# Optimization experiments

Measured on AMD Instinct MI355X. Metric: run time of the kernel, lower is better.

## Reference

```python
import jax, jax.numpy as jnp
import numpy as np

D_IN = 1024
D_OUT = 1024
NUM_HEADS = 16
HEAD_DIM = D_OUT // NUM_HEADS
SEQ = 2048
BATCH = 2


def setup_inputs() -> dict:
    key = jax.random.key(0)
    ks = jax.random.split(key, 6)
    s = 1.0 / np.sqrt(D_IN)
    x = jax.random.normal(ks[0], (BATCH, SEQ, D_IN), dtype=jnp.float32)
    Wq = jax.random.uniform(ks[1], (D_IN, D_OUT), jnp.float32, -s, s)
    Wk = jax.random.uniform(ks[2], (D_IN, D_OUT), jnp.float32, -s, s)
    Wv = jax.random.uniform(ks[3], (D_IN, D_OUT), jnp.float32, -s, s)
    Wo = jax.random.uniform(ks[4], (D_OUT, D_OUT), jnp.float32, -s, s)
    bo = jax.random.uniform(ks[5], (D_OUT,), jnp.float32, -s, s)
    return {"x": x, "Wq": Wq, "Wk": Wk, "Wv": Wv, "Wo": Wo, "bo": bo}


def reference(x, Wq, Wk, Wv, Wo, bo):
    b, n, _ = x.shape
    # projections, split into heads: (b, h, n, hd)
    def split_heads(t):
        return t.reshape(b, n, NUM_HEADS, HEAD_DIM).transpose(0, 2, 1, 3)
    q = split_heads(x @ Wq)
    k = split_heads(x @ Wk)
    v = split_heads(x @ Wv)
    scores = jnp.einsum("bhqd,bhkd->bhqk", q, k)
    causal = jnp.triu(jnp.ones((n, n), dtype=bool), k=1)
    scores = jnp.where(causal, -jnp.inf, scores)
    attn = jax.nn.softmax(scores / np.sqrt(HEAD_DIM), axis=-1)
    # dropout prob is 0.0 -> identity
    ctx = jnp.einsum("bhqk,bhkd->bhqd", attn, v)
    ctx = ctx.transpose(0, 2, 1, 3).reshape(b, n, D_OUT)
    return ctx @ Wo + bo
```

## Files before the change

kernel.cpp:

```cpp
#include <hip/hip_runtime.h>
#include <hip/hip_bf16.h>
#include <stdint.h>

#define D_IN   1024
#define D_OUT  1024
#define NHEAD  16
#define HDIM   64
#define SEQ    2048
#define BATCH  2
#define M_TOT  (BATCH*SEQ)

typedef __attribute__((ext_vector_type(8)))  short bfx8;
typedef __attribute__((ext_vector_type(4)))  short bfx4;
typedef __attribute__((ext_vector_type(4)))  float fx4;
typedef __attribute__((ext_vector_type(16))) float fx16;
typedef unsigned short u16;
typedef unsigned int   u32;

__device__ __forceinline__ u16 f2bf(float f) {
    u32 u = __builtin_bit_cast(u32, f);
    u32 r = (u + 0x7FFFu + ((u >> 16) & 1u)) >> 16;
    return (u16)r;
}

__device__ __forceinline__ u32 cvtpk(float lo, float hi) {
    u32 r;
    asm("v_cvt_pk_bf16_f32 %0, %1, %2" : "=v"(r) : "v"(lo), "v"(hi));
    return r;
}

__device__ __forceinline__ void gload16(const u16* g, u16* l) {
    __builtin_amdgcn_global_load_lds(
        (const __attribute__((address_space(1))) void*)g,
        (__attribute__((address_space(3))) void*)l, 16, 0, 0);
}

__global__ void k_conv_x(const float* __restrict__ x, u16* __restrict__ xb) {
    int i = blockIdx.x * 256 + threadIdx.x;
    const float4* s = reinterpret_cast<const float4*>(x);
    float4 a = s[2*i], b = s[2*i+1];
    uint4 o;
    o.x = (u32)f2bf(a.x) | ((u32)f2bf(a.y) << 16);
    o.y = (u32)f2bf(a.z) | ((u32)f2bf(a.w) << 16);
    o.z = (u32)f2bf(b.x) | ((u32)f2bf(b.y) << 16);
    o.w = (u32)f2bf(b.z) | ((u32)f2bf(b.w) << 16);
    reinterpret_cast<uint4*>(xb)[i] = o;
}

__global__ void k_conv_wt(const float* __restrict__ Wq, const float* __restrict__ Wk,
                          const float* __restrict__ Wv, const float* __restrict__ Wo,
                          u16* __restrict__ wt) {
    __shared__ float tile[32][33];
    int wsel = blockIdx.z;
    const float* W = (wsel == 0) ? Wq : (wsel == 1) ? Wk : (wsel == 2) ? Wv : Wo;
    const float scale = (wsel == 0) ? 0.125f : 1.0f;
    u16* dst = wt + (size_t)wsel * D_IN * D_OUT;
    int r0 = blockIdx.y * 32, c0 = blockIdx.x * 32;
    int tx = threadIdx.x & 31, ty = threadIdx.x >> 5;
    #pragma unroll
    for (int k = 0; k < 4; k++) {
        int i = ty + k * 8;
        tile[i][tx] = W[(size_t)(r0 + i) * D_OUT + c0 + tx];
    }
    __syncthreads();
    #pragma unroll
    for (int k = 0; k < 4; k++) {
        int i = ty + k * 8;
        dst[(size_t)(c0 + i) * D_IN + r0 + tx] = f2bf(tile[tx][i] * scale);
    }
}

template<int MODE>
__global__ __launch_bounds__(256) void k_gemm128(const u16* __restrict__ A,
                                                 const u16* __restrict__ Bt,
                                                 const float* __restrict__ bias,
                                                 u16* __restrict__ outb,
                                                 float* __restrict__ outf) {
    __shared__ u16 aL[128][32];
    __shared__ u16 bL[128][32];
    const int K = 1024;
    const int nb = blockIdx.x * 128, mb = blockIdx.y * 128;
    const int t = threadIdx.x, lane = t & 63, w = t >> 6;
    const int wr = w >> 1, wc = w & 1;
    const int li = lane & 15, lg = lane >> 4;
    const int srow = lane >> 2, schunk = (lane & 3) * 8;

    fx4 acc[4][4];
    #pragma unroll
    for (int i = 0; i < 4; i++)
        #pragma unroll
        for (int j = 0; j < 4; j++) acc[i][j] = fx4{0.f, 0.f, 0.f, 0.f};

    const u16* aBase = A  + (size_t)(mb + w * 32 + srow) * K + schunk;
    const u16* bBase = Bt + (size_t)(nb + w * 32 + srow) * K + schunk;

    for (int kb = 0; kb < K; kb += 32) {
        #pragma unroll
        for (int c = 0; c < 2; c++) {
            gload16(aBase + (size_t)c * 16 * K + kb, &aL[w * 32 + c * 16][0]);
            gload16(bBase + (size_t)c * 16 * K + kb, &bL[w * 32 + c * 16][0]);
        }
        __syncthreads();
        bfx8 af[4], bf[4];
        #pragma unroll
        for (int mi = 0; mi < 4; mi++)
            af[mi] = *reinterpret_cast<const bfx8*>(&aL[wr * 64 + mi * 16 + li][lg * 8]);
        #pragma unroll
        for (int ni = 0; ni < 4; ni++)
            bf[ni] = *reinterpret_cast<const bfx8*>(&bL[wc * 64 + ni * 16 + li][lg * 8]);
        #pragma unroll
        for (int mi = 0; mi < 4; mi++)
            #pragma unroll
            for (int ni = 0; ni < 4; ni++)
                acc[mi][ni] = __builtin_amdgcn_mfma_f32_16x16x32_bf16(af[mi], bf[ni], acc[mi][ni], 0, 0, 0);
        __syncthreads();
    }

    #pragma unroll
    for (int mi = 0; mi < 4; mi++) {
        #pragma unroll
        for (int ni = 0; ni < 4; ni++) {
            const int n = nb + wc * 64 + ni * 16 + li;
            const int m0 = mb + wr * 64 + mi * 16 + lg * 4;
            if (MODE == 0) {
                const int proj = n >> 10, h = (n >> 6) & 15, d = n & 63;
                const int b = m0 >> 11, s0 = m0 & 2047;
                if (proj == 2) {
                    u16* op = outb + (size_t)2 * M_TOT * D_OUT +
                              ((size_t)(b * NHEAD + h) * HDIM + d) * SEQ + s0;
                    bfx4 pk = {(short)f2bf(acc[mi][ni][0]), (short)f2bf(acc[mi][ni][1]),
                               (short)f2bf(acc[mi][ni][2]), (short)f2bf(acc[mi][ni][3])};
                    *reinterpret_cast<bfx4*>(op) = pk;
                } else {
                    u16* op = outb + (size_t)proj * M_TOT * D_OUT;
                    #pragma unroll
                    for (int r = 0; r < 4; r++)
                        op[((size_t)(b * NHEAD + h) * SEQ + s0 + r) * HDIM + d] =
                            f2bf(acc[mi][ni][r]);
                }
            } else {
                const float bv = bias[n];
                #pragma unroll
                for (int r = 0; r < 4; r++)
                    outf[(size_t)(m0 + r) * D_OUT + n] = acc[mi][ni][r] + bv;
            }
        }
    }
}

__global__ __launch_bounds__(128, 2) void k_attn(const u16* __restrict__ Q,
                                                 const u16* __restrict__ Kp,
                                                 const u16* __restrict__ Vt,
                                                 u16* __restrict__ ctx) {
    __shared__ u16 kbuf[2][64][64];
    __shared__ u16 vbuf[2][64][64];

    const int g    = blockIdx.x;
    const int pid  = g & 255, half = g >> 8;
    const int bh   = pid & 31, jb = pid >> 5;
    const int qi   = (half == 0) ? jb : (half == 1) ? (31 - jb)
                   : (half == 2) ? (8 + jb) : (23 - jb);
    const int ntk  = qi + 1;

    const size_t base = (size_t)bh * SEQ * HDIM;
    const int t = threadIdx.x, lane = t & 63, w = t >> 6;
    const int l31 = lane & 31, hi = lane >> 5;
    const int srow = lane >> 3;
    const int ts = (lane & 7) ^ srow;
    const int bq = bh >> 4, hh = bh & 15;
    const int swz = (l31 & 7) * 8;
    const int qwb = qi * 64 + w * 32;
    const int qg  = qwb + l31;

    auto stage = [&](int bi, int kvb) {
        #pragma unroll
        for (int i = 0; i < 4; i++) {
            const int rb = w * 32 + i * 8;
            const int rr = rb + srow;
            gload16(Kp + base + (size_t)(kvb + rr) * HDIM + ts * 8, &kbuf[bi][rb][0]);
            gload16(Vt + base + (size_t)rr * SEQ + kvb + ts * 8,    &vbuf[bi][rb][0]);
        }
    };

    bfx8 qf[4];
    #pragma unroll
    for (int dc = 0; dc < 4; dc++)
        qf[dc] = *reinterpret_cast<const bfx8*>(
            &Q[base + (size_t)qg * HDIM + dc * 16 + hi * 8]);
    fx16 cacc[2];
    #pragma unroll
    for (int dt = 0; dt < 2; dt++)
        #pragma unroll
        for (int r = 0; r < 16; r++) cacc[dt][r] = 0.f;
    float lsum = 0.f;

    stage(0, 0);

    for (int ti = 0; ti < ntk; ti++) {
        if (ti + 1 < ntk) {
            stage((ti + 1) & 1, (ti + 1) * 64);
            asm volatile("s_waitcnt vmcnt(8)" ::: "memory");
        } else {
            asm volatile("s_waitcnt vmcnt(0)" ::: "memory");
        }
        __builtin_amdgcn_s_barrier();
        __builtin_amdgcn_sched_barrier(0);
        const int bi = ti & 1, kvb = ti * 64;
        fx16 sc[2];
        #pragma unroll
        for (int s = 0; s < 2; s++) {
            #pragma unroll
            for (int r = 0; r < 16; r++) sc[s][r] = 0.f;
            #pragma unroll
            for (int dc = 0; dc < 4; dc++) {
                bfx8 kf = *reinterpret_cast<const bfx8*>(
                    &kbuf[bi][s * 32 + l31][(dc * 16 + hi * 8) ^ swz]);
                sc[s] = __builtin_amdgcn_mfma_f32_32x32x16_bf16(kf, qf[dc], sc[s], 0, 0, 0);
            }
        }
        if (kvb + 63 > qwb) {
            #pragma unroll
            for (int s = 0; s < 2; s++)
                #pragma unroll
                for (int r = 0; r < 16; r++) {
                    int kvg = kvb + s * 32 + (r & 3) + 8 * (r >> 2) + 4 * hi;
                    if (kvg > qg) sc[s][r] = -1e30f;
                }
        }
        float ps = 0.f;
        #pragma unroll
        for (int s = 0; s < 2; s++)
            #pragma unroll
            for (int r = 0; r < 16; r++) {
                float pv = __expf(sc[s][r]);
                sc[s][r] = pv;
                ps += pv;
            }
        lsum += ps;
        #pragma unroll
        for (int c = 0; c < 4; c++) {
            const int s = c >> 1, rb = (c & 1) * 8;
            u32 a0 = cvtpk(sc[s][rb + 0], sc[s][rb + 1]);
            u32 a1 = cvtpk(sc[s][rb + 2], sc[s][rb + 3]);
            u32 b0 = cvtpk(sc[s][rb + 4], sc[s][rb + 5]);
            u32 b1 = cvtpk(sc[s][rb + 6], sc[s][rb + 7]);
            u32 X0 = hi ? a0 : b0, X1 = hi ? a1 : b1;
            u32 Y0 = (u32)__shfl_xor((int)X0, 32);
            u32 Y1 = (u32)__shfl_xor((int)X1, 32);
            uint4 pw;
            pw.x = hi ? Y0 : a0;
            pw.y = hi ? Y1 : a1;
            pw.z = hi ? b0 : Y0;
            pw.w = hi ? b1 : Y1;
            bfx8 pf = __builtin_bit_cast(bfx8, pw);
            #pragma unroll
            for (int dt = 0; dt < 2; dt++) {
                bfx8 vf = *reinterpret_cast<const bfx8*>(
                    &vbuf[bi][dt * 32 + l31][(c * 16 + hi * 8) ^ swz]);
                cacc[dt] = __builtin_amdgcn_mfma_f32_32x32x16_bf16(pf, vf, cacc[dt], 0, 0, 0);
            }
        }
        asm volatile("s_waitcnt lgkmcnt(0)" ::: "memory");
        __builtin_amdgcn_s_barrier();
    }

    float ltot = lsum + __shfl_xor(lsum, 32);
    float linv = 1.0f / ltot;
    #pragma unroll
    for (int r = 0; r < 16; r++) {
        const int qpat = (r & 3) + 8 * (r >> 2) + 4 * hi;
        float rl = __shfl(linv, qpat);
        const int q = qwb + qpat;
        #pragma unroll
        for (int dt = 0; dt < 2; dt++)
            ctx[((size_t)(bq * SEQ + q)) * D_OUT + hh * HDIM + dt * 32 + l31] =
                f2bf(cacc[dt][r] * rl);
    }
}

extern "C" void kernel_launch(void* const* d_in, const int* in_sizes, int n_in,
                              void* d_out, int out_size, void* d_ws, size_t ws_size,
                              hipStream_t stream) {
    const float* x  = (const float*)d_in[0];
    const float* Wq = (const float*)d_in[1];
    const float* Wk = (const float*)d_in[2];
    const float* Wv = (const float*)d_in[3];
    const float* Wo = (const float*)d_in[4];
    const float* bo = (const float*)d_in[5];
    float* out = (float*)d_out;

    char* ws = (char*)d_ws;
    u16* xb   = (u16*)(ws);
    u16* wt   = (u16*)(ws + (8u << 20));
    u16* qkvb = (u16*)(ws + (16u << 20));
    u16* ctxb = (u16*)(ws + (40u << 20));

    const u16* Qb  = qkvb;
    const u16* Kb  = qkvb + (size_t)M_TOT * D_OUT;
    const u16* Vtb = qkvb + (size_t)2 * M_TOT * D_OUT;

    k_conv_x <<<2048, 256, 0, stream>>>(x, xb);
    k_conv_wt<<<dim3(32, 32, 4), 256, 0, stream>>>(Wq, Wk, Wv, Wo, wt);
    k_gemm128<0><<<dim3(24, 32), 256, 0, stream>>>(xb, wt, nullptr, qkvb, nullptr);
    k_attn   <<<dim3(1024), 128, 0, stream>>>(Qb, Kb, Vtb, ctxb);
    k_gemm128<1><<<dim3(8, 32), 256, 0, stream>>>(
        ctxb, wt + (size_t)3 * D_IN * D_OUT, bo, nullptr, out);
}
```

Baseline: 115.8 us.

## Split KV range of long causal query blocks into two partial blocks plus combine

Query blocks in the second half of the sequence (qi ≥ 16) now have their KV tiles split across two workgroups. The first part writes its unnormalised bf16 context into ctx and the second writes to a scratch buffer, each with its row sums. A new k_comb kernel adds the two partials and divides by the total sum. This caps per-block work at about 16 tiles to shorten the causal-imbalance tail. In exchange it adds a kernel launch, extra global traffic, and bf16 rounding of the unnormalised partials; the scratch buffers reuse the no-longer-needed xb workspace.

```diff
diff --git a/kernel.cpp b/kernel.cpp
--- a/kernel.cpp
+++ b/kernel.cpp
@@ -21,6 +21,10 @@
     u32 u = __builtin_bit_cast(u32, f);
     u32 r = (u + 0x7FFFu + ((u >> 16) & 1u)) >> 16;
     return (u16)r;
+}
+__device__ __forceinline__ float bf2f(u16 v) {
+    u32 u = (u32)v << 16;
+    return __builtin_bit_cast(float, u);
 }
 
 __device__ __forceinline__ u32 cvtpk(float lo, float hi) {
@@ -151,16 +155,32 @@
 __global__ __launch_bounds__(128, 2) void k_attn(const u16* __restrict__ Q,
                                                  const u16* __restrict__ Kp,
                                                  const u16* __restrict__ Vt,
-                                                 u16* __restrict__ ctx) {
+                                                 u16* __restrict__ ctx,
+                                                 u16* __restrict__ o1,
+                                                 float* __restrict__ l0,
+                                                 float* __restrict__ l1) {
     __shared__ u16 kbuf[2][64][64];
     __shared__ u16 vbuf[2][64][64];
 
-    const int g    = blockIdx.x;
-    const int pid  = g & 255, half = g >> 8;
-    const int bh   = pid & 31, jb = pid >> 5;
-    const int qi   = (half == 0) ? jb : (half == 1) ? (31 - jb)
-                   : (half == 2) ? (8 + jb) : (23 - jb);
-    const int ntk  = qi + 1;
+    const int g = blockIdx.x;
+    int qi, part, m;
+    const bool heavy = (g < 1024);
+    if (heavy) {
+        qi = 31 - (g >> 6);
+        part = (g >> 5) & 1;
+        m = g & 31;
+    } else {
+        int j = g - 1024;
+        qi = 15 - (j >> 5);
+        part = 0;
+        m = j & 31;
+    }
+    const int bh = (m & 7) * 4 + (m >> 3);
+    const int nt = qi + 1;
+    int t0, t1;
+    if (heavy) { int h1 = nt >> 1; t0 = part ? h1 : 0; t1 = part ? nt : h1; }
+    else       { t0 = 0; t1 = nt; }
+    const int ntL = t1 - t0;
 
     const size_t base = (size_t)bh * SEQ * HDIM;
     const int t = threadIdx.x, lane = t & 63, w = t >> 6;
@@ -194,18 +214,19 @@
         for (int r = 0; r < 16; r++) cacc[dt][r] = 0.f;
     float lsum = 0.f;
 
-    stage(0, 0);
-
-    for (int ti = 0; ti < ntk; ti++) {
-        if (ti + 1 < ntk) {
-            stage((ti + 1) & 1, (ti + 1) * 64);
+    stage(0, t0 * 64);
+
+    for (int tt = 0; tt < ntL; tt++) {
+        const int ti = t0 + tt;
+        if (tt + 1 < ntL) {
+            stage((tt + 1) & 1, (ti + 1) * 64);
             asm volatile("s_waitcnt vmcnt(8)" ::: "memory");
         } else {
             asm volatile("s_waitcnt vmcnt(0)" ::: "memory");
         }
         __builtin_amdgcn_s_barrier();
         __builtin_amdgcn_sched_barrier(0);
-        const int bi = ti & 1, kvb = ti * 64;
+        const int bi = tt & 1, kvb = ti * 64;
         fx16 sc[2];
         #pragma unroll
         for (int s = 0; s < 2; s++) {
@@ -265,17 +286,58 @@
     }
 
     float ltot = lsum + __shfl_xor(lsum, 32);
-    float linv = 1.0f / ltot;
-    #pragma unroll
-    for (int r = 0; r < 16; r++) {
-        const int qpat = (r & 3) + 8 * (r >> 2) + 4 * hi;
-        float rl = __shfl(linv, qpat);
-        const int q = qwb + qpat;
-        #pragma unroll
-        for (int dt = 0; dt < 2; dt++)
-            ctx[((size_t)(bq * SEQ + q)) * D_OUT + hh * HDIM + dt * 32 + l31] =
-                f2bf(cacc[dt][r] * rl);
-    }
+    if (!heavy) {
+        float linv = 1.0f / ltot;
+        #pragma unroll
+        for (int r = 0; r < 16; r++) {
+            const int qpat = (r & 3) + 8 * (r >> 2) + 4 * hi;
+            float rl = __shfl(linv, qpat);
+            const int q = qwb + qpat;
+            #pragma unroll
+            for (int dt = 0; dt < 2; dt++)
+                ctx[((size_t)(bq * SEQ + q)) * D_OUT + hh * HDIM + dt * 32 + l31] =
+                    f2bf(cacc[dt][r] * rl);
+        }
+    } else {
+        const int qi16 = qi - 16;
+        const int lidx = ((qi16 * 32 + bh) * 64) + w * 32 + l31;
+        if (hi == 0) { (part ? l1 : l0)[lidx] = ltot; }
+        #pragma unroll
+        for (int r = 0; r < 16; r++) {
+            const int qpat = (r & 3) + 8 * (r >> 2) + 4 * hi;
+            const int q = qwb + qpat;
+            #pragma unroll
+            for (int dt = 0; dt < 2; dt++) {
+                const int d = dt * 32 + l31;
+                u16 val = f2bf(cacc[dt][r]);
+                if (part == 0)
+                    ctx[((size_t)(bq * SEQ + q)) * D_OUT + hh * HDIM + d] = val;
+                else
+                    o1[(((size_t)(qi16 * 32 + bh) * 64) + w * 32 + qpat) * 64 + d] = val;
+            }
+        }
+    }
+}
+
+__global__ void k_comb(u16* __restrict__ ctx, const u16* __restrict__ o1,
+                       const float* __restrict__ l0, const float* __restrict__ l1) {
+    int i = blockIdx.x * 256 + threadIdx.x;
+    const int d    = (i & 7) * 8;
+    const int qrow = (i >> 3) & 63;
+    const int bi_  = i >> 9;
+    const int bh   = bi_ & 31, qi16 = bi_ >> 5;
+    const int bq = bh >> 4, hh = bh & 15;
+    const int token = bq * SEQ + (16 + qi16) * 64 + qrow;
+    const size_t cidx = (size_t)token * D_OUT + hh * HDIM + d;
+    const size_t oidx = ((size_t)(bi_ * 64 + qrow)) * 64 + d;
+    const float linv = 1.0f / (l0[bi_ * 64 + qrow] + l1[bi_ * 64 + qrow]);
+    bfx8 a = *reinterpret_cast<const bfx8*>(&ctx[cidx]);
+    bfx8 b = *reinterpret_cast<const bfx8*>(&o1[oidx]);
+    bfx8 o;
+    #pragma unroll
+    for (int j = 0; j < 8; j++)
+        o[j] = (short)f2bf((bf2f((u16)a[j]) + bf2f((u16)b[j])) * linv);
+    *reinterpret_cast<bfx8*>(&ctx[cidx]) = o;
 }
 
 extern "C" void kernel_launch(void* const* d_in, const int* in_sizes, int n_in,
@@ -295,6 +357,10 @@
     u16* qkvb = (u16*)(ws + (16u << 20));
     u16* ctxb = (u16*)(ws + (40u << 20));
 
+    u16*   o1p = (u16*)(ws);
+    float* l0p = (float*)(ws + (4u << 20));
+    float* l1p = (float*)(ws + (4u << 20) + (128u << 10));
+
     const u16* Qb  = qkvb;
     const u16* Kb  = qkvb + (size_t)M_TOT * D_OUT;
     const u16* Vtb = qkvb + (size_t)2 * M_TOT * D_OUT;
@@ -302,7 +368,8 @@
     k_conv_x <<<2048, 256, 0, stream>>>(x, xb);
     k_conv_wt<<<dim3(32, 32, 4), 256, 0, stream>>>(Wq, Wk, Wv, Wo, wt);
     k_gemm128<0><<<dim3(24, 32), 256, 0, stream>>>(xb, wt, nullptr, qkvb, nullptr);
-    k_attn   <<<dim3(1024), 128, 0, stream>>>(Qb, Kb, Vtb, ctxb);
+    k_attn   <<<dim3(1536), 128, 0, stream>>>(Qb, Kb, Vtb, ctxb, o1p, l0p, l1p);
+    k_comb   <<<1024, 256, 0, stream>>>(ctxb, o1p, l0p, l1p);
     k_gemm128<1><<<dim3(8, 32), 256, 0, stream>>>(
         ctxb, wt + (size_t)3 * D_IN * D_OUT, bo, nullptr, out);
 }
```

New measurement: 116.1 us. About the same (+0.2%).
